# Performance work log

Measured on AMD Instinct MI355X. Metric: run time of the kernel, lower is better.

Reference implementation:

```python
import jax, jax.numpy as jnp
import numpy as np

N, H, A, D = 16384, 50, 16, 64
VU, VV, R = 100000, 100000, 8
REL_TOK = R - 1  # relation_token
K_SELECT = 33    # max(1, int(percent * L)) with percent=0.5, L=H+A=66


def setup_inputs() -> dict:
    key = jax.random.key(0)
    ks = jax.random.split(key, 11)
    return {
        "self_feats": jax.random.normal(ks[0], (N, D), jnp.float32),
        "target_feats": jax.random.normal(ks[1], (N, D), jnp.float32),
        "history_uv": jax.random.randint(ks[2], (N, H), 0, VU),
        "history_r": jax.random.randint(ks[3], (N, H), 0, R),
        "adj": jax.random.randint(ks[4], (N, A), 0, VV),
        "u2e_w": jax.random.normal(ks[5], (VU, D), jnp.float32),
        "v2e_w": jax.random.normal(ks[6], (VV, D), jnp.float32),
        "r2e_w": jax.random.normal(ks[7], (R, D), jnp.float32),
        "relation_att": jax.random.normal(ks[8], (2 * D,), jnp.float32),
        "W": jax.random.normal(ks[9], (2 * D, D), jnp.float32) / np.sqrt(2 * D),
        "b": jnp.zeros((D,), jnp.float32),
        "k_select": K_SELECT,
    }


def reference(self_feats, target_feats, u2e_w, v2e_w, r2e_w,
              relation_att, W, b, history_uv, history_r, adj, k_select):
    # uv=True branch: history rows index the user table, adj rows the item table.
    e_uv = jnp.concatenate([u2e_w[history_uv], v2e_w[adj]], axis=1)        # [N, L, D]
    labels = jnp.concatenate(
        [history_r, jnp.full(adj.shape, REL_TOK, history_r.dtype)], axis=1)  # [N, L]
    e_r = r2e_w[labels]                                                     # [N, L, D]

    # query = Linear(cat(self, target))
    query = jnp.concatenate([self_feats, target_feats], axis=-1) @ W + b    # [N, D]

    # prob = softmax(-||query - neighbors||); multinomial w/o replacement
    # == Gumbel-top-k on the logits (-dist); the softmax normalizer is a
    # per-node constant so we add Gumbel noise to -dist directly.
    dist = jnp.linalg.norm(query[:, None, :] - e_uv, axis=-1)               # [N, L]
    u = jax.random.uniform(jax.random.key(42), dist.shape, jnp.float32, 1e-20, 1.0)
    gumbel = -jnp.log(-jnp.log(u))
    _, idx = jax.lax.top_k(-dist + gumbel, k_select)                        # [N, K]

    sel_n = jnp.take_along_axis(e_uv, idx[..., None], axis=1)               # [N, K, D]
    sel_r = jnp.take_along_axis(e_r, idx[..., None], axis=1)                # [N, K, D]

    # cat(neighbor, relation) @ relation_att -> attention logits
    att = sel_n @ relation_att[:D] + sel_r @ relation_att[D:]               # [N, K]
    w_att = jax.nn.softmax(att, axis=1)
    return jnp.einsum('nkd,nk->nd', sel_n, w_att)                           # [N, D]
```

## Files before the change

### kernel.cpp

```cpp
#include <hip/hip_runtime.h>
#include <math.h>

#define NN 16384
#define HH 50
#define AA 16
#define LL 66
#define RELTOK 7

__device__ __forceinline__ unsigned rotl32(unsigned x, int d){
  return (x << d) | (x >> (32 - d));
}
__device__ __forceinline__ void tfr(unsigned &x0, unsigned &x1, int r){
  x0 += x1; x1 = rotl32(x1, r); x1 ^= x0;
}
__device__ float gumbel_at(unsigned j){
  const unsigned k0 = 0u, k1 = 42u;
  const unsigned k2 = 0x1BD11BDAu ^ k0 ^ k1;
  unsigned x0 = 0u + k0;
  unsigned x1 = j  + k1;
  tfr(x0,x1,13); tfr(x0,x1,15); tfr(x0,x1,26); tfr(x0,x1,6);
  x0 += k1; x1 += k2 + 1u;
  tfr(x0,x1,17); tfr(x0,x1,29); tfr(x0,x1,16); tfr(x0,x1,24);
  x0 += k2; x1 += k0 + 2u;
  tfr(x0,x1,13); tfr(x0,x1,15); tfr(x0,x1,26); tfr(x0,x1,6);
  x0 += k0; x1 += k1 + 3u;
  tfr(x0,x1,17); tfr(x0,x1,29); tfr(x0,x1,16); tfr(x0,x1,24);
  x0 += k1; x1 += k2 + 4u;
  tfr(x0,x1,13); tfr(x0,x1,15); tfr(x0,x1,26); tfr(x0,x1,6);
  x0 += k2; x1 += k0 + 5u;
  const unsigned bits = x0 ^ x1;
  const float f = __uint_as_float((bits >> 9) | 0x3F800000u) - 1.0f;
  const float u = fmaxf(f + 1e-20f, 1e-20f);
  return -logf(-logf(u));
}

__global__ void size_sentinel(float* out, int code){
  if (threadIdx.x < 64) out[threadIdx.x] = 3000.f + (float)code;
}
__global__ void kcheck_kernel(const int* kPtr, float* out){
  if (kPtr[0] != 33 && threadIdx.x < 64)
    out[threadIdx.x] = 5000.f + (float)kPtr[0];
}

__global__ __launch_bounds__(256) void query_kernel(
    const float* __restrict__ selfF, const float* __restrict__ targF,
    const float* __restrict__ W, const float* __restrict__ bvec,
    float* __restrict__ qout)
{
  __shared__ float lw[128*64];
  const int tid = threadIdx.x;
  for (int i = tid; i < 128*64; i += 256) lw[i] = W[i];
  __syncthreads();
  const int lane = tid & 63;
  const int wv = tid >> 6;
  const int base = blockIdx.x * 16 + wv * 4;
  for (int r = 0; r < 4; ++r){
    const int n = base + r;
    const float sv = selfF[(size_t)n*64 + lane];
    const float tv = targF[(size_t)n*64 + lane];
    float q = bvec[lane];
    #pragma unroll
    for (int k = 0; k < 64; ++k)
      q = fmaf(__shfl(sv, k), lw[k*64 + lane], q);
    #pragma unroll
    for (int k = 0; k < 64; ++k)
      q = fmaf(__shfl(tv, k), lw[(64+k)*64 + lane], q);
    qout[(size_t)n*64 + lane] = q;
  }
}

__global__ __launch_bounds__(64) void node_agg(
    const int* __restrict__ histUV, const int* __restrict__ histR,
    const int* __restrict__ adj,
    const float* __restrict__ u2e, const float* __restrict__ v2e,
    const float* __restrict__ r2e, const float* __restrict__ relAtt,
    const float* __restrict__ qbuf,
    const int* __restrict__ kPtr, float* __restrict__ out)
{
  __shared__ float ras[128];
  __shared__ float lrel[8];
  __shared__ float qs[64];
  __shared__ float Gum[66];
  __shared__ int   Didx[66];
  __shared__ int   Dlab[66];
  __shared__ float Dlog[66];
  __shared__ float Datt[66];
  __shared__ float Dw[66];
  __shared__ int   DnI[66];
  __shared__ float Cw[40];
  __shared__ int   Cn[40];

  const int lane = threadIdx.x;
  const int n = blockIdx.x;
  const int K = kPtr[0];

  ras[lane]      = relAtt[lane];
  ras[64 + lane] = relAtt[64 + lane];
  {
    const float rh = relAtt[64 + lane];
    #pragma unroll
    for (int r = 0; r < 8; ++r){
      float v = r2e[r*64 + lane] * rh;
      #pragma unroll
      for (int o = 1; o < 64; o <<= 1) v += __shfl_xor(v, o);
      if (lane == 0) lrel[r] = v;
    }
  }
  qs[lane] = qbuf[(size_t)n*64 + lane];

  if (lane < HH){
    Didx[lane] = histUV[(size_t)n*HH + lane];
    Dlab[lane] = histR[(size_t)n*HH + lane];
  } else {
    Didx[lane] = adj[(size_t)n*AA + (lane - HH)];
    Dlab[lane] = RELTOK;
  }
  Gum[lane] = gumbel_at((unsigned)(n*LL + lane));
  if (lane < 2){
    Didx[64 + lane] = adj[(size_t)n*AA + 14 + lane];
    Dlab[64 + lane] = RELTOK;
    Gum[64 + lane] = gumbel_at((unsigned)(n*LL + 64 + lane));
  }
  __syncthreads();

  {
    const int g  = lane >> 4;
    const int li = lane & 15;
    const float4 q4  = *reinterpret_cast<const float4*>(&qs[4*li]);
    const float4 ra4 = *reinterpret_cast<const float4*>(&ras[4*li]);
    #pragma unroll
    for (int j = 0; j < 17; ++j){
      const int l = 4*j + g;
      if (j < 16 || g < 2){
        const int idx = Didx[l];
        const float* tbl = (l < HH) ? u2e : v2e;
        const float4 ev = *(reinterpret_cast<const float4*>(tbl + (size_t)idx*64) + li);
        const float d0 = q4.x - ev.x;
        const float d1 = q4.y - ev.y;
        const float d2 = q4.z - ev.z;
        const float d3 = q4.w - ev.w;
        float s = fmaf(d0,d0, fmaf(d1,d1, fmaf(d2,d2, d3*d3)));
        float e = fmaf(ev.x,ra4.x, fmaf(ev.y,ra4.y, fmaf(ev.z,ra4.z, ev.w*ra4.w)));
        #pragma unroll
        for (int o = 1; o < 16; o <<= 1){
          s += __shfl_xor(s, o);
          e += __shfl_xor(e, o);
        }
        if (li == 0){
          Dlog[l] = Gum[l] - sqrtf(s);
          Datt[l] = e + lrel[Dlab[l]];
          DnI[l]  = idx | ((l < HH) ? 0 : (1 << 30));
        }
      }
    }
  }
  __syncthreads();

  for (int rep = 0; rep < 2; ++rep){
    const int l = (rep == 0) ? lane : 64 + lane;
    if (l < LL && (rep == 0 || lane < 2)){
      const float v = Dlog[l];
      int r = 0;
      for (int m = 0; m < LL; ++m){
        const float lm = Dlog[m];
        r += (lm > v || (lm == v && m < l)) ? 1 : 0;
      }
      Dw[l] = (r < K) ? 1.f : 0.f;
    }
  }
  __syncthreads();

  {
    const float a0 = Datt[lane];
    const bool  s0 = Dw[lane] > 0.f;
    float a1 = 0.f; bool s1 = false;
    if (lane < 2){ a1 = Datt[64 + lane]; s1 = Dw[64 + lane] > 0.f; }
    float mx = s0 ? a0 : -INFINITY;
    if (s1) mx = fmaxf(mx, a1);
    #pragma unroll
    for (int o = 1; o < 64; o <<= 1) mx = fmaxf(mx, __shfl_xor(mx, o));
    const float e0 = s0 ? expf(a0 - mx) : 0.f;
    const float e1 = s1 ? expf(a1 - mx) : 0.f;
    float ss = e0 + e1;
    #pragma unroll
    for (int o = 1; o < 64; o <<= 1) ss += __shfl_xor(ss, o);
    const float inv = 1.0f / ss;
    Dw[lane] = e0 * inv;
    if (lane < 2) Dw[64 + lane] = e1 * inv;
  }
  __syncthreads();

  int M;
  {
    if (lane < 40){ Cw[lane] = 0.f; Cn[lane] = 0; }
    const float w = Dw[lane];
    const bool sel = (w > 0.f);
    const unsigned long long mask = __ballot(sel);
    const int pos = __popcll(mask & ((1ull << lane) - 1ull));
    if (sel){ Cw[pos] = w; Cn[pos] = DnI[lane]; }
    const int base = __popcll(mask);
    const bool s64 = Dw[64] > 0.f;
    const bool s65 = Dw[65] > 0.f;
    if (lane == 0 && s64){ Cw[base] = Dw[64]; Cn[base] = DnI[64]; }
    if (lane == 1 && s65){
      const int tp = base + (s64 ? 1 : 0);
      Cw[tp] = Dw[65]; Cn[tp] = DnI[65];
    }
    M = base + (s64 ? 1 : 0) + (s65 ? 1 : 0);
  }
  __syncthreads();

  float od = 0.f;
  if (M <= 36){
    #pragma unroll
    for (int i = 0; i < 36; ++i){
      const float w = Cw[i];
      const int enc = Cn[i];
      const float* tbl = (enc & (1 << 30)) ? v2e : u2e;
      od = fmaf(w, tbl[(size_t)(enc & 0x3FFFFFFF)*64 + lane], od);
    }
  } else {
    for (int i = 0; i < M; ++i){
      const float w = Cw[i];
      const int enc = Cn[i];
      const float* tbl = (enc & (1 << 30)) ? v2e : u2e;
      od = fmaf(w, tbl[(size_t)(enc & 0x3FFFFFFF)*64 + lane], od);
    }
  }
  out[(size_t)n*64 + lane] = od;
}

__global__ __launch_bounds__(256) void node_agg_dumb(
    const float* __restrict__ selfF, const float* __restrict__ targF,
    const int* __restrict__ histUV, const int* __restrict__ histR,
    const int* __restrict__ adj,
    const float* __restrict__ u2e, const float* __restrict__ v2e,
    const float* __restrict__ r2e, const float* __restrict__ relAtt,
    const float* __restrict__ W, const float* __restrict__ bvec,
    const int* __restrict__ kPtr, float* __restrict__ out)
{
  __shared__ float lw[128*64];
  __shared__ float ras[128];
  __shared__ float lrel[8];
  __shared__ float cs[4][128];
  __shared__ float qs[4][64];
  __shared__ float Dlog[4][66];
  __shared__ float Datt[4][66];
  __shared__ float Dw[4][66];
  __shared__ int   DnI[4][66];

  const int tid = threadIdx.x;
  for (int i = tid; i < 128*64; i += 256) lw[i] = W[i];
  if (tid < 128) ras[tid] = relAtt[tid];
  if (tid < 64){
    const float rh = relAtt[64 + tid];
    #pragma unroll
    for (int r = 0; r < 8; ++r){
      float v = r2e[r*64 + tid] * rh;
      #pragma unroll
      for (int o = 1; o < 64; o <<= 1) v += __shfl_xor(v, o);
      if (tid == 0) lrel[r] = v;
    }
  }
  __syncthreads();

  const int lane = tid & 63;
  const int wv = tid >> 6;
  const int n = blockIdx.x * 4 + wv;
  const int K = kPtr[0];

  cs[wv][lane]      = selfF[(size_t)n*64 + lane];
  cs[wv][64 + lane] = targF[(size_t)n*64 + lane];
  __syncthreads();
  {
    float qd = bvec[lane];
    for (int k = 0; k < 128; ++k) qd = fmaf(cs[wv][k], lw[k*64 + lane], qd);
    qs[wv][lane] = qd;
  }
  __syncthreads();
  for (int rep = 0; rep < 2; ++rep){
    const int l = (rep == 0) ? lane : 64 + lane;
    if (l < LL && (rep == 0 || lane < 2)){
      int idx, lab;
      if (l < HH){ idx = histUV[(size_t)n*HH + l]; lab = histR[(size_t)n*HH + l]; }
      else       { idx = adj[(size_t)n*AA + (l - HH)]; lab = RELTOK; }
      const float* row = ((l < HH) ? u2e : v2e) + (size_t)idx*64;
      float s = 0.f, e = 0.f;
      for (int d = 0; d < 64; ++d){
        const float ev = row[d];
        const float df = qs[wv][d] - ev;
        s = fmaf(df, df, s);
        e = fmaf(ev, ras[d], e);
      }
      Dlog[wv][l] = gumbel_at((unsigned)(n*LL + l)) - sqrtf(s);
      Datt[wv][l] = e + lrel[lab];
      DnI[wv][l]  = idx | ((l < HH) ? 0 : (1 << 30));
    }
  }
  __syncthreads();
  for (int rep = 0; rep < 2; ++rep){
    const int l = (rep == 0) ? lane : 64 + lane;
    if (l < LL && (rep == 0 || lane < 2)){
      const float v = Dlog[wv][l];
      int r = 0;
      for (int m = 0; m < LL; ++m){
        const float lm = Dlog[wv][m];
        r += (lm > v || (lm == v && m < l)) ? 1 : 0;
      }
      Dw[wv][l] = (r < K) ? 1.f : 0.f;
    }
  }
  __syncthreads();
  if (lane == 0){
    float mx = -INFINITY;
    for (int l = 0; l < LL; ++l) if (Dw[wv][l] > 0.f) mx = fmaxf(mx, Datt[wv][l]);
    float ss = 0.f;
    for (int l = 0; l < LL; ++l){
      const float w = (Dw[wv][l] > 0.f) ? expf(Datt[wv][l] - mx) : 0.f;
      Dw[wv][l] = w; ss += w;
    }
    const float inv = 1.f / ss;
    for (int l = 0; l < LL; ++l) Dw[wv][l] *= inv;
  }
  __syncthreads();
  float od = 0.f;
  for (int l = 0; l < LL; ++l){
    const float w = Dw[wv][l];
    if (w != 0.f){
      const int enc = DnI[wv][l];
      const float* tbl = (enc & (1 << 30)) ? v2e : u2e;
      od = fmaf(w, tbl[(size_t)(enc & 0x3FFFFFFF)*64 + lane], od);
    }
  }
  out[(size_t)n*64 + lane] = od;
}

extern "C" void kernel_launch(void* const* d_in, const int* in_sizes, int n_in,
                              void* d_out, int out_size, void* d_ws, size_t ws_size,
                              hipStream_t stream)
{
  float* out = (float*)d_out;

  static const int exp_sizes[12] = {1048576, 1048576, 819200, 819200, 262144,
                                    6400000, 6400000, 512, 128, 8192, 64, 1};
  int bad = -1;
  if (n_in != 12) bad = 99;
  else {
    for (int i = 0; i < 12; ++i){
      if (in_sizes[i] != exp_sizes[i]){ bad = i; break; }
    }
  }
  if (bad >= 0){
    size_sentinel<<<1, 64, 0, stream>>>(out, bad);
    return;
  }

  const float* selfF  = (const float*)d_in[0];
  const float* targF  = (const float*)d_in[1];
  const int*   histUV = (const int*)d_in[2];
  const int*   histR  = (const int*)d_in[3];
  const int*   adj    = (const int*)d_in[4];
  const float* u2e    = (const float*)d_in[5];
  const float* v2e    = (const float*)d_in[6];
  const float* r2e    = (const float*)d_in[7];
  const float* relAtt = (const float*)d_in[8];
  const float* W      = (const float*)d_in[9];
  const float* bvec   = (const float*)d_in[10];
  const int*   kPtr   = (const int*)d_in[11];

  const size_t qbytes = (size_t)NN * 64 * sizeof(float);
  if (ws_size >= qbytes){
    float* qbuf = (float*)d_ws;
    query_kernel<<<NN/16, 256, 0, stream>>>(selfF, targF, W, bvec, qbuf);
    node_agg<<<NN, 64, 0, stream>>>(histUV, histR, adj, u2e, v2e, r2e,
                                    relAtt, qbuf, kPtr, out);
  } else {
    node_agg_dumb<<<NN/4, 256, 0, stream>>>(selfF, targF, histUV, histR, adj,
                                            u2e, v2e, r2e, relAtt, W, bvec,
                                            kPtr, out);
  }
  kcheck_kernel<<<1, 64, 0, stream>>>(kPtr, out);
}
```

Before: 101.7 us.

## Keep gathered neighbor embeddings in registers and reuse them for weighted sum

```diff
diff --git a/kernel.cpp b/kernel.cpp
--- a/kernel.cpp
+++ b/kernel.cpp
@@ -86,9 +86,6 @@
   __shared__ float Dlog[66];
   __shared__ float Datt[66];
   __shared__ float Dw[66];
-  __shared__ int   DnI[66];
-  __shared__ float Cw[40];
-  __shared__ int   Cn[40];
 
   const int lane = threadIdx.x;
   const int n = blockIdx.x;
@@ -123,34 +120,40 @@
   }
   __syncthreads();
 
-  {
-    const int g  = lane >> 4;
-    const int li = lane & 15;
-    const float4 q4  = *reinterpret_cast<const float4*>(&qs[4*li]);
-    const float4 ra4 = *reinterpret_cast<const float4*>(&ras[4*li]);
-    #pragma unroll
-    for (int j = 0; j < 17; ++j){
-      const int l = 4*j + g;
-      if (j < 16 || g < 2){
-        const int idx = Didx[l];
-        const float* tbl = (l < HH) ? u2e : v2e;
-        const float4 ev = *(reinterpret_cast<const float4*>(tbl + (size_t)idx*64) + li);
-        const float d0 = q4.x - ev.x;
-        const float d1 = q4.y - ev.y;
-        const float d2 = q4.z - ev.z;
-        const float d3 = q4.w - ev.w;
-        float s = fmaf(d0,d0, fmaf(d1,d1, fmaf(d2,d2, d3*d3)));
-        float e = fmaf(ev.x,ra4.x, fmaf(ev.y,ra4.y, fmaf(ev.z,ra4.z, ev.w*ra4.w)));
-        #pragma unroll
-        for (int o = 1; o < 16; o <<= 1){
-          s += __shfl_xor(s, o);
-          e += __shfl_xor(e, o);
-        }
-        if (li == 0){
-          Dlog[l] = Gum[l] - sqrtf(s);
-          Datt[l] = e + lrel[Dlab[l]];
-          DnI[l]  = idx | ((l < HH) ? 0 : (1 << 30));
-        }
+  const int g  = lane >> 4;
+  const int li = lane & 15;
+  const float4 q4  = *reinterpret_cast<const float4*>(&qs[4*li]);
+  const float4 ra4 = *reinterpret_cast<const float4*>(&ras[4*li]);
+
+  float4 ev[17];
+  #pragma unroll
+  for (int j = 0; j < 17; ++j){
+    const int l  = 4*j + g;
+    const int lc = (l < LL) ? l : g;
+    const int idx = Didx[lc];
+    const float* tbl = (lc < HH) ? u2e : v2e;
+    ev[j] = *(reinterpret_cast<const float4*>(tbl + (size_t)idx*64) + li);
+  }
+
+  #pragma unroll
+  for (int j = 0; j < 17; ++j){
+    const int l = 4*j + g;
+    if (l < LL){
+      const float4 e4 = ev[j];
+      const float d0 = q4.x - e4.x;
+      const float d1 = q4.y - e4.y;
+      const float d2 = q4.z - e4.z;
+      const float d3 = q4.w - e4.w;
+      float s = fmaf(d0,d0, fmaf(d1,d1, fmaf(d2,d2, d3*d3)));
+      float e = fmaf(e4.x,ra4.x, fmaf(e4.y,ra4.y, fmaf(e4.z,ra4.z, e4.w*ra4.w)));
+      #pragma unroll
+      for (int o = 1; o < 16; o <<= 1){
+        s += __shfl_xor(s, o);
+        e += __shfl_xor(e, o);
+      }
+      if (li == 0){
+        Dlog[l] = Gum[l] - sqrtf(s);
+        Datt[l] = e + lrel[Dlab[l]];
       }
     }
   }
@@ -190,44 +193,26 @@
   }
   __syncthreads();
 
-  int M;
-  {
-    if (lane < 40){ Cw[lane] = 0.f; Cn[lane] = 0; }
-    const float w = Dw[lane];
-    const bool sel = (w > 0.f);
-    const unsigned long long mask = __ballot(sel);
-    const int pos = __popcll(mask & ((1ull << lane) - 1ull));
-    if (sel){ Cw[pos] = w; Cn[pos] = DnI[lane]; }
-    const int base = __popcll(mask);
-    const bool s64 = Dw[64] > 0.f;
-    const bool s65 = Dw[65] > 0.f;
-    if (lane == 0 && s64){ Cw[base] = Dw[64]; Cn[base] = DnI[64]; }
-    if (lane == 1 && s65){
-      const int tp = base + (s64 ? 1 : 0);
-      Cw[tp] = Dw[65]; Cn[tp] = DnI[65];
-    }
-    M = base + (s64 ? 1 : 0) + (s65 ? 1 : 0);
-  }
-  __syncthreads();
-
-  float od = 0.f;
-  if (M <= 36){
-    #pragma unroll
-    for (int i = 0; i < 36; ++i){
-      const float w = Cw[i];
-      const int enc = Cn[i];
-      const float* tbl = (enc & (1 << 30)) ? v2e : u2e;
-      od = fmaf(w, tbl[(size_t)(enc & 0x3FFFFFFF)*64 + lane], od);
-    }
-  } else {
-    for (int i = 0; i < M; ++i){
-      const float w = Cw[i];
-      const int enc = Cn[i];
-      const float* tbl = (enc & (1 << 30)) ? v2e : u2e;
-      od = fmaf(w, tbl[(size_t)(enc & 0x3FFFFFFF)*64 + lane], od);
-    }
-  }
-  out[(size_t)n*64 + lane] = od;
+  float4 acc = make_float4(0.f, 0.f, 0.f, 0.f);
+  #pragma unroll
+  for (int j = 0; j < 17; ++j){
+    const int l = 4*j + g;
+    const float w = (l < LL) ? Dw[l] : 0.f;
+    acc.x = fmaf(w, ev[j].x, acc.x);
+    acc.y = fmaf(w, ev[j].y, acc.y);
+    acc.z = fmaf(w, ev[j].z, acc.z);
+    acc.w = fmaf(w, ev[j].w, acc.w);
+  }
+  #pragma unroll
+  for (int o = 16; o < 64; o <<= 1){
+    acc.x += __shfl_xor(acc.x, o);
+    acc.y += __shfl_xor(acc.y, o);
+    acc.z += __shfl_xor(acc.z, o);
+    acc.w += __shfl_xor(acc.w, o);
+  }
+  if (g == 0){
+    *reinterpret_cast<float4*>(out + (size_t)n*64 + 4*li) = acc;
+  }
 }
 
 __global__ __launch_bounds__(256) void node_agg_dumb(
```

Result: no change. 103.2 us (+1.5%).
